# Optimization experiments

Hardware: AMD Instinct MI355X
Metric: run time of the kernel (lower is better)

Reference implementation:

```python
import jax, jax.numpy as jnp
import numpy as np

B, T, D, HS = 4, 4096, 1024, 64


def setup_inputs() -> dict:
    key = jax.random.key(0)
    k1, k2, k3 = jax.random.split(key, 3)
    x = jax.random.normal(k1, (B, T, D), dtype=jnp.float32)
    # Linear(n_embd, head_size, bias=False) weights: [head_size, n_embd]
    Wk = jax.random.normal(k2, (HS, D), dtype=jnp.float32) * (D ** -0.5)
    Wv = jax.random.normal(k3, (HS, D), dtype=jnp.float32) * (D ** -0.5)
    return {"x": x, "Wk": Wk, "Wv": Wv}


def reference(x, Wk, Wv):
    # Faithful to source: q = self.value(x) (query proj is dead code), so q and v
    # share the value projection.
    k = jnp.einsum('btd,hd->bth', x, Wk)   # [B,T,HS]
    qv = jnp.einsum('btd,hd->bth', x, Wv)  # [B,T,HS]; serves as both q and v
    scale = k.shape[-1] ** -0.5
    scores = jnp.einsum('bth,bsh->bts', qv, k) * scale  # [B,T,T]
    causal = jnp.tril(jnp.ones((T, T), dtype=bool))
    scores = jnp.where(causal, scores, -jnp.inf)
    weights = jax.nn.softmax(scores, axis=-1)
    out = jnp.einsum('bts,bsh->bth', weights, qv)  # [B,T,HS]
    return out
```

## Files before the change

kernel.cpp:

```cpp
#include <hip/hip_runtime.h>
#include <hip/hip_bf16.h>

typedef __bf16 bf16;
typedef __attribute__((ext_vector_type(4))) __bf16 bf16x4;
typedef __attribute__((ext_vector_type(8))) __bf16 bf16x8;
typedef __attribute__((ext_vector_type(4))) float f32x4;

#define T_SEQ 4096
#define D_EMB 1024
#define HS 64

__device__ __forceinline__ float fexp2(float x) {
#if __has_builtin(__builtin_amdgcn_exp2f)
    return __builtin_amdgcn_exp2f(x);
#else
    return exp2f(x);
#endif
}

__global__ __launch_bounds__(256) void wcast_kernel(
    const float* __restrict__ Wk, const float* __restrict__ Wv,
    bf16* __restrict__ wbf)
{
    const int t = blockIdx.x * 256 + threadIdx.x;
    const int base = t * 8;
    const float* src = (base < 65536) ? (Wk + base) : (Wv + base - 65536);
    float4 f0 = *(const float4*)(src);
    float4 f1 = *(const float4*)(src + 4);
    bf16x8 o = {(__bf16)f0.x, (__bf16)f0.y, (__bf16)f0.z, (__bf16)f0.w,
                (__bf16)f1.x, (__bf16)f1.y, (__bf16)f1.z, (__bf16)f1.w};
    *(bf16x8*)(wbf + base) = o;
}

__global__ __launch_bounds__(256, 4) void proj_kernel(
    const float* __restrict__ x,
    const bf16* __restrict__ wbf,
    float* __restrict__ pbuf)
{
    __shared__ bf16 xs[32][72];
    __shared__ bf16 wsh[128][72];

    const int tid  = threadIdx.x;
    const int lane = tid & 63;
    const int wave = tid >> 6;
    const int col  = lane & 15;
    const int quad = lane >> 4;

    const int mb = blockIdx.x & 511;
    const int kh = blockIdx.x >> 9;
    const int rowbase = mb * 32;
    const int kbase   = kh * 512;

    f32x4 acc[2][2];
#pragma unroll
    for (int mt = 0; mt < 2; ++mt)
#pragma unroll
        for (int nt = 0; nt < 2; ++nt) acc[mt][nt] = {0.f, 0.f, 0.f, 0.f};

    float4 xn[2];
    bf16x8 wn[4];
    {
#pragma unroll
        for (int p = 0; p < 2; ++p) {
            const int idx = p * 256 + tid;
            const int xr  = idx >> 4;
            const int c4  = (idx & 15) * 4;
            xn[p] = *(const float4*)(x + (size_t)(rowbase + xr) * D_EMB + kbase + c4);
        }
#pragma unroll
        for (int p = 0; p < 4; ++p) {
            const int idx = p * 256 + tid;
            const int wr  = idx >> 3;
            const int off = (idx & 7) * 8;
            wn[p] = *(const bf16x8*)(wbf + (size_t)wr * D_EMB + kbase + off);
        }
    }

#pragma unroll 1
    for (int c = 0; c < 8; ++c) {
#pragma unroll
        for (int p = 0; p < 2; ++p) {
            const int idx = p * 256 + tid;
            const int xr  = idx >> 4;
            const int c4  = (idx & 15) * 4;
            bf16x4 v = {(__bf16)xn[p].x, (__bf16)xn[p].y,
                        (__bf16)xn[p].z, (__bf16)xn[p].w};
            *(bf16x4*)&xs[xr][c4] = v;
        }
#pragma unroll
        for (int p = 0; p < 4; ++p) {
            const int idx = p * 256 + tid;
            const int wr  = idx >> 3;
            const int off = (idx & 7) * 8;
            *(bf16x8*)&wsh[wr][off] = wn[p];
        }
        __syncthreads();

        if (c < 7) {
            const int k0 = kbase + (c + 1) * 64;
#pragma unroll
            for (int p = 0; p < 2; ++p) {
                const int idx = p * 256 + tid;
                const int xr  = idx >> 4;
                const int c4  = (idx & 15) * 4;
                xn[p] = *(const float4*)(x + (size_t)(rowbase + xr) * D_EMB + k0 + c4);
            }
#pragma unroll
            for (int p = 0; p < 4; ++p) {
                const int idx = p * 256 + tid;
                const int wr  = idx >> 3;
                const int off = (idx & 7) * 8;
                wn[p] = *(const bf16x8*)(wbf + (size_t)wr * D_EMB + k0 + off);
            }
        }

#pragma unroll
        for (int s = 0; s < 2; ++s) {
            bf16x8 af[2];
#pragma unroll
            for (int mt = 0; mt < 2; ++mt)
                af[mt] = *(const bf16x8*)&xs[mt * 16 + col][s * 32 + quad * 8];
            bf16x8 bfr[2];
#pragma unroll
            for (int nt = 0; nt < 2; ++nt)
                bfr[nt] = *(const bf16x8*)&wsh[wave * 32 + nt * 16 + col][s * 32 + quad * 8];
#pragma unroll
            for (int mt = 0; mt < 2; ++mt)
#pragma unroll
                for (int nt = 0; nt < 2; ++nt)
                    acc[mt][nt] = __builtin_amdgcn_mfma_f32_16x16x32_bf16(
                        af[mt], bfr[nt], acc[mt][nt], 0, 0, 0);
        }
        __syncthreads();
    }

    float* ph = pbuf + (size_t)kh * 16384 * 128;
#pragma unroll
    for (int mt = 0; mt < 2; ++mt)
#pragma unroll
        for (int nt = 0; nt < 2; ++nt) {
            const int gcol = wave * 32 + nt * 16 + col;
#pragma unroll
            for (int r = 0; r < 4; ++r) {
                const int grow = rowbase + mt * 16 + quad * 4 + r;
                ph[(size_t)grow * 128 + gcol] = acc[mt][nt][r];
            }
        }
}

__global__ __launch_bounds__(256) void pcomb_kernel(
    const float* __restrict__ pbuf,
    bf16* __restrict__ kmat,
    bf16* __restrict__ qvmat,
    bf16* __restrict__ qvT)
{
    const int g   = blockIdx.x * 256 + threadIdx.x;
    const int row = g >> 4;
    const int cg  = g & 15;
    const size_t base = (size_t)row * 128 + cg * 8;

    f32x4 a0 = *(const f32x4*)(pbuf + base);
    f32x4 a1 = *(const f32x4*)(pbuf + base + 4);
    f32x4 b0 = *(const f32x4*)(pbuf + (size_t)16384 * 128 + base);
    f32x4 b1 = *(const f32x4*)(pbuf + (size_t)16384 * 128 + base + 4);
    a0 += b0; a1 += b1;
    bf16x8 v = {(__bf16)a0[0], (__bf16)a0[1], (__bf16)a0[2], (__bf16)a0[3],
                (__bf16)a1[0], (__bf16)a1[1], (__bf16)a1[2], (__bf16)a1[3]};

    if (cg < 8) {
        *(bf16x8*)(kmat + (size_t)row * HS + cg * 8) = v;
    } else {
        const int h0 = (cg - 8) * 8;
        *(bf16x8*)(qvmat + (size_t)row * HS + h0) = v;
        const int bb = row >> 12;
        const int tt = row & (T_SEQ - 1);
#pragma unroll
        for (int j = 0; j < 8; ++j)
            qvT[((size_t)bb * HS + h0 + j) * T_SEQ + tt] = v[j];
    }
}

__global__ __launch_bounds__(256, 5) void attn_kernel(
    const bf16* __restrict__ kmat,
    const bf16* __restrict__ qvmat,
    const bf16* __restrict__ qvT,
    float* __restrict__ out,
    float* __restrict__ o_parts,
    float* __restrict__ l_parts)
{
    __shared__ bf16 Kt[64][72];
    __shared__ bf16 Vt[64][72];
    __shared__ bf16 plds[4][16][40];

    const int tid  = threadIdx.x;
    const int lane = tid & 63;
    const int wave = tid >> 6;
    const int col  = lane & 15;
    const int quad = lane >> 4;

    const int b = blockIdx.x / 288;
    const int r = 287 - (blockIdx.x - b * 288);
    int a = 0;
    while (4 * (a + 1) * (a + 2) <= r) ++a;
    const int rr = r - 4 * a * (a + 1);
    const int m  = rr / (a + 1);
    const int jc = rr - m * (a + 1);
    const int qb = 8 * a + m;

    const int cbeg  = jc * 8;
    const int nctot = qb + 1;
    const int cend  = (nctot < cbeg + 8) ? nctot : cbeg + 8;

    const bf16* qvb = qvmat + (size_t)b * T_SEQ * HS;
    const bf16* kb  = kmat  + (size_t)b * T_SEQ * HS;
    const bf16* vTb = qvT   + (size_t)b * HS * T_SEQ;

    const int q0 = qb * 64 + wave * 16;

    bf16x8 qf0 = *(const bf16x8*)(qvb + (size_t)(q0 + col) * HS + quad * 8);
    bf16x8 qf1 = *(const bf16x8*)(qvb + (size_t)(q0 + col) * HS + 32 + quad * 8);

    f32x4 o[4];
    float lp[4];
#pragma unroll
    for (int h = 0; h < 4; ++h) o[h] = {0.f, 0.f, 0.f, 0.f};
#pragma unroll
    for (int i = 0; i < 4; ++i) lp[i] = 0.f;

    const float sc = 0.125f * 1.44269504088896f;

    bf16x8 kn[2], vn[2];
    {
        const int kc = cbeg * 64;
#pragma unroll
        for (int it = 0; it < 2; ++it) {
            const int idx = it * 256 + tid;
            const int kr  = idx >> 3;
            const int off = (idx & 7) * 8;
            kn[it] = *(const bf16x8*)(kb + (size_t)kc * HS + idx * 8);
            vn[it] = *(const bf16x8*)(vTb + (size_t)kr * T_SEQ + kc + off);
        }
    }

#pragma unroll 1
    for (int c = cbeg; c < cend; ++c) {
#pragma unroll
        for (int it = 0; it < 2; ++it) {
            const int idx = it * 256 + tid;
            const int kr  = idx >> 3;
            const int off = (idx & 7) * 8;
            *(bf16x8*)&Kt[kr][off] = kn[it];
            *(bf16x8*)&Vt[kr][off] = vn[it];
        }
        __syncthreads();

        if (c + 1 < cend) {
            const int kcn = (c + 1) * 64;
#pragma unroll
            for (int it = 0; it < 2; ++it) {
                const int idx = it * 256 + tid;
                const int kr  = idx >> 3;
                const int off = (idx & 7) * 8;
                kn[it] = *(const bf16x8*)(kb + (size_t)kcn * HS + idx * 8);
                vn[it] = *(const bf16x8*)(vTb + (size_t)kr * T_SEQ + kcn + off);
            }
        }

        const int kc = c * 64;
#pragma unroll
        for (int st = 0; st < 2; ++st) {
            const int gk = kc + 32 * st;
            if (gk > q0 + 15) break;

            bf16x8 b0 = *(const bf16x8*)&Kt[32 * st + col][quad * 8];
            bf16x8 b1 = *(const bf16x8*)&Kt[32 * st + col][32 + quad * 8];
            bf16x8 b2 = *(const bf16x8*)&Kt[32 * st + 16 + col][quad * 8];
            bf16x8 b3 = *(const bf16x8*)&Kt[32 * st + 16 + col][32 + quad * 8];

            float p[2][4];
            {
                f32x4 a4 = {0.f, 0.f, 0.f, 0.f};
                a4 = __builtin_amdgcn_mfma_f32_16x16x32_bf16(qf0, b0, a4, 0, 0, 0);
                a4 = __builtin_amdgcn_mfma_f32_16x16x32_bf16(qf1, b1, a4, 0, 0, 0);
#pragma unroll
                for (int i = 0; i < 4; ++i) p[0][i] = fexp2(fmaf(a4[i], sc, -24.f));
            }
            {
                f32x4 a4 = {0.f, 0.f, 0.f, 0.f};
                a4 = __builtin_amdgcn_mfma_f32_16x16x32_bf16(qf0, b2, a4, 0, 0, 0);
                a4 = __builtin_amdgcn_mfma_f32_16x16x32_bf16(qf1, b3, a4, 0, 0, 0);
#pragma unroll
                for (int i = 0; i < 4; ++i) p[1][i] = fexp2(fmaf(a4[i], sc, -24.f));
            }

            if (gk + 31 > q0) {
#pragma unroll
                for (int nt = 0; nt < 2; ++nt)
#pragma unroll
                    for (int i = 0; i < 4; ++i)
                        if (gk + nt * 16 + col > q0 + quad * 4 + i)
                            p[nt][i] = 0.f;
            }

#pragma unroll
            for (int i = 0; i < 4; ++i) lp[i] += p[0][i] + p[1][i];

#pragma unroll
            for (int nt = 0; nt < 2; ++nt)
#pragma unroll
                for (int i = 0; i < 4; ++i)
                    plds[wave][quad * 4 + i][nt * 16 + col] = (bf16)p[nt][i];
            bf16x8 pa = *(const bf16x8*)&plds[wave][col][quad * 8];

#pragma unroll
            for (int h = 0; h < 4; ++h) {
                bf16x8 vb = *(const bf16x8*)&Vt[h * 16 + col][32 * st + quad * 8];
                o[h] = __builtin_amdgcn_mfma_f32_16x16x32_bf16(pa, vb, o[h], 0, 0, 0);
            }
        }
        __syncthreads();
    }

    float lr[4];
#pragma unroll
    for (int i = 0; i < 4; ++i) {
        float v = lp[i];
#pragma unroll
        for (int off = 1; off < 16; off <<= 1)
            v += __shfl_xor(v, off, 64);
        lr[i] = v;
    }

    const size_t rowbase = (size_t)b * T_SEQ + q0 + quad * 4;
    if (col == 0) {
#pragma unroll
        for (int i = 0; i < 4; ++i)
            l_parts[(size_t)jc * 16384 + rowbase + i] = lr[i];
    }

    float* dst = (jc == 0) ? out : (o_parts + (size_t)(jc - 1) * 16384 * HS);
#pragma unroll
    for (int h = 0; h < 4; ++h)
#pragma unroll
        for (int i = 0; i < 4; ++i)
            dst[(rowbase + i) * HS + h * 16 + col] = o[h][i];
}

__global__ __launch_bounds__(256) void norm_kernel(
    float* __restrict__ out,
    const float* __restrict__ o_parts,
    const float* __restrict__ l_parts)
{
    const int i   = blockIdx.x * 256 + threadIdx.x;
    const int row = i >> 6;
    const int qb  = (row & 4095) >> 6;
    const int nj  = (qb >> 3) + 1;

    float s = out[i];
    float L = l_parts[row];
    for (int j = 1; j < nj; ++j) {
        s += o_parts[(size_t)(j - 1) * 1048576 + i];
        L += l_parts[(size_t)j * 16384 + row];
    }
    out[i] = s / L;
}

extern "C" void kernel_launch(void* const* d_in, const int* in_sizes, int n_in,
                              void* d_out, int out_size, void* d_ws, size_t ws_size,
                              hipStream_t stream) {
    const float* x  = (const float*)d_in[0];
    const float* Wk = (const float*)d_in[1];
    const float* Wv = (const float*)d_in[2];
    float* out = (float*)d_out;

    bf16* ws    = (bf16*)d_ws;
    bf16* wbf   = ws;
    bf16* kmat  = ws + (size_t)128 * 1024;
    bf16* qvmat = kmat + (size_t)16384 * 64;
    bf16* qvT   = qvmat + (size_t)16384 * 64;
    float* o_parts = (float*)(qvT + (size_t)16384 * 64);
    float* l_parts = o_parts + (size_t)7 * 16384 * 64;
    float* pbuf    = l_parts + (size_t)8 * 16384;

    wcast_kernel<<<64, 256, 0, stream>>>(Wk, Wv, wbf);
    proj_kernel<<<1024, 256, 0, stream>>>(x, wbf, pbuf);
    pcomb_kernel<<<1024, 256, 0, stream>>>(pbuf, kmat, qvmat, qvT);
    attn_kernel<<<1152, 256, 0, stream>>>(kmat, qvmat, qvT, out, o_parts, l_parts);
    norm_kernel<<<4096, 256, 0, stream>>>(out, o_parts, l_parts);
}
```

Measured before the change: 147.2 us.

## Fuse projection partial-sum combine into proj kernel, drop split-K

The projection no longer splits the D=1024 reduction into two halves written to an fp32 partial buffer. Each block now runs the full reduction and writes bf16 K, QV and a transposed QV directly, staging the transpose through shared memory so the stores are coalesced. This removes the pcomb kernel launch and the fp32 partial-buffer round trip through memory. In exchange only 512 blocks run, each with twice the serial K-loop work, so parallelism is lower. Launch bounds also change: proj's minimum-blocks hint goes from 4 to 2 and attn's from 5 to 4.

Result: faster. 137.6 us (-6.5%).

```diff
diff --git a/kernel.cpp b/kernel.cpp
--- a/kernel.cpp
+++ b/kernel.cpp
@@ -32,24 +32,23 @@
     *(bf16x8*)(wbf + base) = o;
 }
 
-__global__ __launch_bounds__(256, 4) void proj_kernel(
+__global__ __launch_bounds__(256, 2) void proj_kernel(
     const float* __restrict__ x,
     const bf16* __restrict__ wbf,
-    float* __restrict__ pbuf)
+    bf16* __restrict__ kmat,
+    bf16* __restrict__ qvmat,
+    bf16* __restrict__ qvT)
 {
     __shared__ bf16 xs[32][72];
     __shared__ bf16 wsh[128][72];
+    __shared__ bf16 vt[64][40];
 
     const int tid  = threadIdx.x;
     const int lane = tid & 63;
     const int wave = tid >> 6;
     const int col  = lane & 15;
     const int quad = lane >> 4;
-
-    const int mb = blockIdx.x & 511;
-    const int kh = blockIdx.x >> 9;
-    const int rowbase = mb * 32;
-    const int kbase   = kh * 512;
+    const int rowbase = blockIdx.x * 32;
 
     f32x4 acc[2][2];
 #pragma unroll
@@ -65,19 +64,19 @@
             const int idx = p * 256 + tid;
             const int xr  = idx >> 4;
             const int c4  = (idx & 15) * 4;
-            xn[p] = *(const float4*)(x + (size_t)(rowbase + xr) * D_EMB + kbase + c4);
+            xn[p] = *(const float4*)(x + (size_t)(rowbase + xr) * D_EMB + c4);
         }
 #pragma unroll
         for (int p = 0; p < 4; ++p) {
             const int idx = p * 256 + tid;
             const int wr  = idx >> 3;
             const int off = (idx & 7) * 8;
-            wn[p] = *(const bf16x8*)(wbf + (size_t)wr * D_EMB + kbase + off);
+            wn[p] = *(const bf16x8*)(wbf + (size_t)wr * D_EMB + off);
         }
     }
 
 #pragma unroll 1
-    for (int c = 0; c < 8; ++c) {
+    for (int c = 0; c < 16; ++c) {
 #pragma unroll
         for (int p = 0; p < 2; ++p) {
             const int idx = p * 256 + tid;
@@ -96,8 +95,8 @@
         }
         __syncthreads();
 
-        if (c < 7) {
-            const int k0 = kbase + (c + 1) * 64;
+        if (c < 15) {
+            const int k0 = (c + 1) * 64;
 #pragma unroll
             for (int p = 0; p < 2; ++p) {
                 const int idx = p * 256 + tid;
@@ -134,7 +133,6 @@
         __syncthreads();
     }
 
-    float* ph = pbuf + (size_t)kh * 16384 * 128;
 #pragma unroll
     for (int mt = 0; mt < 2; ++mt)
 #pragma unroll
@@ -143,44 +141,29 @@
 #pragma unroll
             for (int r = 0; r < 4; ++r) {
                 const int grow = rowbase + mt * 16 + quad * 4 + r;
-                ph[(size_t)grow * 128 + gcol] = acc[mt][nt][r];
-            }
-        }
-}
-
-__global__ __launch_bounds__(256) void pcomb_kernel(
-    const float* __restrict__ pbuf,
-    bf16* __restrict__ kmat,
-    bf16* __restrict__ qvmat,
-    bf16* __restrict__ qvT)
-{
-    const int g   = blockIdx.x * 256 + threadIdx.x;
-    const int row = g >> 4;
-    const int cg  = g & 15;
-    const size_t base = (size_t)row * 128 + cg * 8;
-
-    f32x4 a0 = *(const f32x4*)(pbuf + base);
-    f32x4 a1 = *(const f32x4*)(pbuf + base + 4);
-    f32x4 b0 = *(const f32x4*)(pbuf + (size_t)16384 * 128 + base);
-    f32x4 b1 = *(const f32x4*)(pbuf + (size_t)16384 * 128 + base + 4);
-    a0 += b0; a1 += b1;
-    bf16x8 v = {(__bf16)a0[0], (__bf16)a0[1], (__bf16)a0[2], (__bf16)a0[3],
-                (__bf16)a1[0], (__bf16)a1[1], (__bf16)a1[2], (__bf16)a1[3]};
-
-    if (cg < 8) {
-        *(bf16x8*)(kmat + (size_t)row * HS + cg * 8) = v;
-    } else {
-        const int h0 = (cg - 8) * 8;
-        *(bf16x8*)(qvmat + (size_t)row * HS + h0) = v;
-        const int bb = row >> 12;
-        const int tt = row & (T_SEQ - 1);
-#pragma unroll
-        for (int j = 0; j < 8; ++j)
-            qvT[((size_t)bb * HS + h0 + j) * T_SEQ + tt] = v[j];
-    }
-}
-
-__global__ __launch_bounds__(256, 5) void attn_kernel(
+                const int ltt  = mt * 16 + quad * 4 + r;
+                bf16 bv = (bf16)acc[mt][nt][r];
+                if (gcol < 64) {
+                    kmat[(size_t)grow * HS + gcol] = bv;
+                } else {
+                    qvmat[(size_t)grow * HS + (gcol - 64)] = bv;
+                    vt[gcol - 64][ltt] = bv;
+                }
+            }
+        }
+    __syncthreads();
+
+    {
+        const int h   = tid >> 2;
+        const int seg = (tid & 3) * 8;
+        bf16x8 v = *(const bf16x8*)&vt[h][seg];
+        const int bb  = rowbase >> 12;
+        const int tt0 = (rowbase & (T_SEQ - 1)) + seg;
+        *(bf16x8*)(qvT + ((size_t)bb * HS + h) * T_SEQ + tt0) = v;
+    }
+}
+
+__global__ __launch_bounds__(256, 4) void attn_kernel(
     const bf16* __restrict__ kmat,
     const bf16* __restrict__ qvmat,
     const bf16* __restrict__ qvT,
@@ -380,11 +363,9 @@
     bf16* qvT   = qvmat + (size_t)16384 * 64;
     float* o_parts = (float*)(qvT + (size_t)16384 * 64);
     float* l_parts = o_parts + (size_t)7 * 16384 * 64;
-    float* pbuf    = l_parts + (size_t)8 * 16384;
 
     wcast_kernel<<<64, 256, 0, stream>>>(Wk, Wv, wbf);
-    proj_kernel<<<1024, 256, 0, stream>>>(x, wbf, pbuf);
-    pcomb_kernel<<<1024, 256, 0, stream>>>(pbuf, kmat, qvmat, qvT);
+    proj_kernel<<<512, 256, 0, stream>>>(x, wbf, kmat, qvmat, qvT);
     attn_kernel<<<1152, 256, 0, stream>>>(kmat, qvmat, qvT, out, o_parts, l_parts);
     norm_kernel<<<4096, 256, 0, stream>>>(out, o_parts, l_parts);
 }
```
